# Optimization experiments

Hardware: AMD Instinct MI355X
Metric: run time of the kernel (lower is better)

## Reference

```python
import jax, jax.numpy as jnp
import numpy as np

# Dimensions (see shape_source): batched instruction states.
B, P, D, H, NOPS = 16384, 8, 64, 128, 37
OP_START = 16            # opcode one-hot lives in channels [16, 16+37)
DIV, MOD = 3, 4          # opcode ids for the iterative div/mod paths
CARRY_OPS = (0, 1, 2, 10, 11, 12, 13)  # ADD,SUB,MUL,LT,GT,LE,GE
NITER = 16               # div/mod iteration FFN count (source: ModuleList of 16)
NCASCADE = 7             # carry cascade iterations (source: for _ in range(7))


def setup_inputs() -> dict:
    key = jax.random.key(0)
    ks = jax.random.split(key, 20)
    s = 0.05
    n = lambda k, shape: jax.random.normal(k, shape, dtype=jnp.float32) * s
    return {
        "x": jax.random.normal(ks[0], (B, P, D), dtype=jnp.float32),
        # initial_experts (per-opcode FFN bank)
        "Wi1": n(ks[1], (NOPS, D, H)), "bi1": jnp.zeros((NOPS, H), jnp.float32),
        "Wi2": n(ks[2], (NOPS, H, D)), "bi2": jnp.zeros((NOPS, D), jnp.float32),
        # carry_attn QKV projections
        "Wq": n(ks[3], (D, D)), "Wk": n(ks[4], (D, D)), "Wv": n(ks[5], (D, D)),
        # carry_experts (per-opcode FFN bank used in the 7-iter cascade)
        "Wc1": n(ks[6], (NOPS, D, H)), "bc1": jnp.zeros((NOPS, H), jnp.float32),
        "Wc2": n(ks[7], (NOPS, H, D)), "bc2": jnp.zeros((NOPS, D), jnp.float32),
        # 16 distinct DivIterFFN layers
        "Wd1": n(ks[8], (NITER, D, H)), "bd1": jnp.zeros((NITER, H), jnp.float32),
        "Wd2": n(ks[9], (NITER, H, D)), "bd2": jnp.zeros((NITER, D), jnp.float32),
        # 16 distinct ModIterFFN layers
        "Wm1": n(ks[10], (NITER, D, H)), "bm1": jnp.zeros((NITER, H), jnp.float32),
        "Wm2": n(ks[11], (NITER, H, D)), "bm2": jnp.zeros((NITER, D), jnp.float32),
        # final_experts (per-opcode FFN bank)
        "Wf1": n(ks[12], (NOPS, D, H)), "bf1": jnp.zeros((NOPS, H), jnp.float32),
        "Wf2": n(ks[13], (NOPS, H, D)), "bf2": jnp.zeros((NOPS, D), jnp.float32),
    }


def _moe(x, op, W1, b1, W2, b2):
    """Opcode-routed expert FFN with residual: each batch element uses its opcode's weights."""
    h = jax.nn.relu(jnp.einsum('bpd,bdh->bph', x, W1[op]) + b1[op][:, None, :])
    return x + jnp.einsum('bph,bhd->bpd', h, W2[op]) + b2[op][:, None, :]


def _attn(x, Wq, Wk, Wv):
    """Carry-propagation attention across the 8 nibble positions, residual."""
    q, k, v = x @ Wq, x @ Wk, x @ Wv
    s = jax.nn.softmax(jnp.einsum('bpd,bqd->bpq', q, k) * (1.0 / np.sqrt(D)), axis=-1)
    return x + jnp.einsum('bpq,bqd->bpd', s, v)


def reference(x, Wi1, bi1, Wi2, bi2, Wq, Wk, Wv, Wc1, bc1, Wc2, bc2,
              Wd1, bd1, Wd2, bd2, Wm1, bm1, Wm2, bm2, Wf1, bf1, Wf2, bf2):
    # opcode routing: argmax over the one-hot opcode slice at position 0
    op = jnp.argmax(x[:, 0, OP_START:OP_START + NOPS], axis=-1)  # [B] int
    # Stage 1: initial opcode-routed experts
    x = _moe(x, op, Wi1, bi1, Wi2, bi2)
    carry_mask = jnp.any(op[:, None] == jnp.asarray(CARRY_OPS)[None, :], axis=1)[:, None, None]
    for _ in range(NCASCADE):
        y = _moe(_attn(x, Wq, Wk, Wv), op, Wc1, bc1, Wc2, bc2)
        x = jnp.where(carry_mask, y, x)
    # 16 iterative DIV FFNs (distinct weights per iteration), masked to DIV rows
    div_mask = (op == DIV)[:, None, None]
    for i in range(NITER):
        h = jax.nn.relu(jnp.einsum('bpd,dh->bph', x, Wd1[i]) + bd1[i])
        x = jnp.where(div_mask, x + jnp.einsum('bph,hd->bpd', h, Wd2[i]) + bd2[i], x)
    # 16 iterative MOD FFNs, masked to MOD rows
    mod_mask = (op == MOD)[:, None, None]
    for i in range(NITER):
        h = jax.nn.relu(jnp.einsum('bpd,dh->bph', x, Wm1[i]) + bm1[i])
        x = jnp.where(mod_mask, x + jnp.einsum('bph,hd->bpd', h, Wm2[i]) + bm2[i], x)
    # Stage 4: finalization experts (opcode-routed)
    x = _moe(x, op, Wf1, bf1, Wf2, bf2)
    return x
```

## Files before the change

### kernel.cpp

```cpp
#include <hip/hip_runtime.h>
#include <math.h>


typedef __bf16 bfrag __attribute__((ext_vector_type(8)));
typedef __bf16 bhalf4 __attribute__((ext_vector_type(4)));
typedef float f32x4 __attribute__((ext_vector_type(4)));

#define MFMA16(a,b,c) __builtin_amdgcn_mfma_f32_16x16x32_bf16((a),(b),(c),0,0,0)

constexpr int NB = 16384, NOPS = 37, OP_START = 16;

constexpr int WS_OPARR  = 0;
constexpr int WS_CNT    = 16384;
constexpr int WS_OFF    = 16448;
constexpr int WS_CUR    = 16512;
constexpr int WS_TB     = 16560;
constexpr int WS_ROWIDX = 16640;
constexpr int WS_INTS   = 33024;

constexpr int OFF_QKVT = 0;
constexpr int OFF_WI1T = 12288;
constexpr int OFF_WI2T = 315392;
constexpr int OFF_WC1T = 618496;
constexpr int OFF_WC2T = 921600;
constexpr int OFF_WF1T = 1224704;
constexpr int OFF_WF2T = 1527808;
constexpr int OFF_WD1T = 1830912;
constexpr int OFF_WD2T = 1961984;
constexpr int OFF_WM1T = 2093056;
constexpr int OFF_WM2T = 2224128;


__global__ void k_zero(int* cnt, int* cur) {
    int t = threadIdx.x;
    if (t < NOPS) { cnt[t] = 0; cur[t] = 0; }
}

__global__ void k_op(const float* __restrict__ x, int* __restrict__ opArr, int* __restrict__ cnt) {
    int b = blockIdx.x * 64 + threadIdx.x;
    const float4* p = (const float4*)(x + (size_t)b * 512 + OP_START);
    float best = -1e30f; int op = 0;
    #pragma unroll
    for (int j = 0; j < 9; ++j) {
        float4 v = p[j];
        int k = j * 4;
        if (v.x > best) { best = v.x; op = k; }
        if (v.y > best) { best = v.y; op = k + 1; }
        if (v.z > best) { best = v.z; op = k + 2; }
        if (v.w > best) { best = v.w; op = k + 3; }
    }
    float last = x[(size_t)b * 512 + OP_START + 36];
    if (last > best) op = 36;
    opArr[b] = op;
    atomicAdd(&cnt[op], 1);
}

__global__ void k_scan(const int* __restrict__ cnt, int* __restrict__ off, int* __restrict__ tb) {
    if (threadIdx.x == 0) {
        int a = 0;
        for (int o = 0; o < NOPS; ++o) { off[o] = a; a += cnt[o]; }
        off[NOPS] = a;
        const int pr[9] = {3, 4, 0, 1, 2, 10, 11, 12, 13};
        int t = 0;
        for (int i = 0; i < 9; ++i) { int o = pr[i]; tb[o] = t; t += (cnt[o] + 3) >> 2; }
        for (int o = 0; o < NOPS; ++o) {
            bool heavy = (o <= 4) || (o >= 10 && o <= 13);
            if (heavy) continue;
            tb[o] = t; t += (cnt[o] + 3) >> 2;
        }
        tb[NOPS] = t;
    }
}

__global__ void k_scatter(const int* __restrict__ opArr, const int* __restrict__ off,
                          int* __restrict__ cur, int* __restrict__ rowIdx) {
    __shared__ int h[NOPS], bb[NOPS];
    int tid = threadIdx.x;
    if (tid < NOPS) h[tid] = 0;
    __syncthreads();
    int b = blockIdx.x * 256 + tid;
    int op = opArr[b];
    int my = atomicAdd(&h[op], 1);
    __syncthreads();
    if (tid < NOPS && h[tid] > 0) bb[tid] = atomicAdd(&cur[tid], h[tid]);
    __syncthreads();
    rowIdx[off[op] + bb[op] + my] = b;
}

__global__ void k_tilemap(const int* __restrict__ cnt, const int* __restrict__ tb,
                          int* __restrict__ tileArr) {
    int o = blockIdx.x;
    int n = (cnt[o] + 3) >> 2, base = tb[o];
    for (int t = threadIdx.x; t < n; t += 64)
        tileArr[base + t] = (o << 12) | t;
}

__global__ void k_wt(const float* __restrict__ Wi1, const float* __restrict__ Wi2,
                     const float* __restrict__ Wq,  const float* __restrict__ Wk,
                     const float* __restrict__ Wv,
                     const float* __restrict__ Wc1, const float* __restrict__ Wc2,
                     const float* __restrict__ Wd1, const float* __restrict__ Wd2,
                     const float* __restrict__ Wm1, const float* __restrict__ Wm2,
                     const float* __restrict__ Wf1, const float* __restrict__ Wf2,
                     __bf16* __restrict__ wb) {
    __shared__ float t[8320];
    int m = blockIdx.x;
    const float* src; __bf16* dst; int R, C;
    if      (m < 37)  { src = Wi1 + m * 8192;        dst = wb + OFF_WI1T + m * 8192;        R = 64;  C = 128; }
    else if (m < 74)  { src = Wi2 + (m-37) * 8192;   dst = wb + OFF_WI2T + (m-37) * 8192;   R = 128; C = 64;  }
    else if (m < 111) { src = Wc1 + (m-74) * 8192;   dst = wb + OFF_WC1T + (m-74) * 8192;   R = 64;  C = 128; }
    else if (m < 148) { src = Wc2 + (m-111) * 8192;  dst = wb + OFF_WC2T + (m-111) * 8192;  R = 128; C = 64;  }
    else if (m < 185) { src = Wf1 + (m-148) * 8192;  dst = wb + OFF_WF1T + (m-148) * 8192;  R = 64;  C = 128; }
    else if (m < 222) { src = Wf2 + (m-185) * 8192;  dst = wb + OFF_WF2T + (m-185) * 8192;  R = 128; C = 64;  }
    else if (m < 238) { src = Wd1 + (m-222) * 8192;  dst = wb + OFF_WD1T + (m-222) * 8192;  R = 64;  C = 128; }
    else if (m < 254) { src = Wd2 + (m-238) * 8192;  dst = wb + OFF_WD2T + (m-238) * 8192;  R = 128; C = 64;  }
    else if (m < 270) { src = Wm1 + (m-254) * 8192;  dst = wb + OFF_WM1T + (m-254) * 8192;  R = 64;  C = 128; }
    else if (m < 286) { src = Wm2 + (m-270) * 8192;  dst = wb + OFF_WM2T + (m-270) * 8192;  R = 128; C = 64;  }
    else { const float* q3[3] = {Wq, Wk, Wv}; src = q3[m-286]; dst = wb + OFF_QKVT + (m-286) * 4096; R = 64; C = 64; }
    int n = R * C, Cp = C + 1;
    int logC = (C == 128) ? 7 : 6, logR = (R == 128) ? 7 : 6;
    for (int i = threadIdx.x; i < n; i += 256)
        t[(i >> logC) * Cp + (i & (C - 1))] = src[i];
    __syncthreads();
    for (int o = threadIdx.x; o < n; o += 256) {
        int c = o >> logR, r = o & (R - 1);
        dst[o] = (__bf16)t[r * Cp + c];
    }
}


__device__ __forceinline__ bfrag cvt8(const float* p) {
    float4 a = *(const float4*)p;
    float4 b = *(const float4*)(p + 4);
    bfrag r;
    r[0] = (__bf16)a.x; r[1] = (__bf16)a.y; r[2] = (__bf16)a.z; r[3] = (__bf16)a.w;
    r[4] = (__bf16)b.x; r[5] = (__bf16)b.y; r[6] = (__bf16)b.z; r[7] = (__bf16)b.w;
    return r;
}

__device__ __forceinline__ bhalf4 pack4(f32x4 a) {
    bhalf4 r;
    r[0] = (__bf16)a[0]; r[1] = (__bf16)a[1]; r[2] = (__bf16)a[2]; r[3] = (__bf16)a[3];
    return r;
}

__device__ __forceinline__ bhalf4 pack4_relu(f32x4 a) {
    bhalf4 r;
    r[0] = (__bf16)fmaxf(a[0], 0.0f); r[1] = (__bf16)fmaxf(a[1], 0.0f);
    r[2] = (__bf16)fmaxf(a[2], 0.0f); r[3] = (__bf16)fmaxf(a[3], 0.0f);
    return r;
}

__device__ __forceinline__ void ffn_coop(float* Xs, __bf16* Hs,
    const __bf16* __restrict__ W1t, const float* __restrict__ b1,
    const __bf16* __restrict__ W2t, const float* __restrict__ b2,
    int w, int lq, int qd) {
    __syncthreads();
    {
        bfrag xa[2][2];
        #pragma unroll
        for (int mt = 0; mt < 2; ++mt)
            #pragma unroll
            for (int kf = 0; kf < 2; ++kf)
                xa[mt][kf] = cvt8(&Xs[(mt * 16 + lq) * 68 + kf * 32 + qd * 8]);
        #pragma unroll
        for (int nt2 = 0; nt2 < 2; ++nt2) {
            int nt = w * 2 + nt2;
            float4 bv = *(const float4*)(b1 + nt * 16 + qd * 4);
            f32x4 acc0 = {bv.x, bv.y, bv.z, bv.w}, acc1 = acc0;
            #pragma unroll
            for (int kf = 0; kf < 2; ++kf) {
                bfrag wf = *(const bfrag*)(W1t + (nt * 16 + lq) * 64 + kf * 32 + qd * 8);
                acc0 = MFMA16(wf, xa[0][kf], acc0);
                acc1 = MFMA16(wf, xa[1][kf], acc1);
            }
            *(bhalf4*)&Hs[lq * 136 + nt * 16 + qd * 4]        = pack4_relu(acc0);
            *(bhalf4*)&Hs[(16 + lq) * 136 + nt * 16 + qd * 4] = pack4_relu(acc1);
        }
    }
    __syncthreads();
    {
        float4 bv = *(const float4*)(b2 + w * 16 + qd * 4);
        f32x4 acc0 = {bv.x, bv.y, bv.z, bv.w}, acc1 = acc0;
        #pragma unroll
        for (int kf = 0; kf < 4; ++kf) {
            bfrag wf = *(const bfrag*)(W2t + (w * 16 + lq) * 128 + kf * 32 + qd * 8);
            bfrag h0 = *(const bfrag*)&Hs[lq * 136 + kf * 32 + qd * 8];
            bfrag h1 = *(const bfrag*)&Hs[(16 + lq) * 136 + kf * 32 + qd * 8];
            acc0 = MFMA16(wf, h0, acc0);
            acc1 = MFMA16(wf, h1, acc1);
        }
        float4* p0 = (float4*)&Xs[lq * 68 + w * 16 + qd * 4];
        float4 v0 = *p0;
        v0.x += acc0[0]; v0.y += acc0[1]; v0.z += acc0[2]; v0.w += acc0[3];
        *p0 = v0;
        float4* p1 = (float4*)&Xs[(16 + lq) * 68 + w * 16 + qd * 4];
        float4 v1 = *p1;
        v1.x += acc1[0]; v1.y += acc1[1]; v1.z += acc1[2]; v1.w += acc1[3];
        *p1 = v1;
    }
}

__device__ __forceinline__ void attn_coop(float* Xs, __bf16* Qb, __bf16* Kb,
    __bf16* VtT, __bf16* Pb, const __bf16* __restrict__ qkvt, int w, int lq, int qd) {
    int c = w >> 1, half = w & 1;
    __syncthreads();
    {
        bfrag xa[2];
        #pragma unroll
        for (int kf = 0; kf < 2; ++kf)
            xa[kf] = cvt8(&Xs[(c * 16 + lq) * 68 + kf * 32 + qd * 8]);
        int nt0 = half * 6;
        #pragma unroll
        for (int i = 0; i < 6; ++i) {
            int nt = nt0 + i;
            f32x4 acc = {0.f, 0.f, 0.f, 0.f};
            if (nt < 8) {
                #pragma unroll
                for (int kf = 0; kf < 2; ++kf) {
                    bfrag wf = *(const bfrag*)(qkvt + (nt * 16 + lq) * 64 + kf * 32 + qd * 8);
                    acc = MFMA16(wf, xa[kf], acc);
                }
                __bf16* dst = (nt < 4)
                    ? &Qb[c * 1280 + lq * 80 + nt * 16 + qd * 4]
                    : &Kb[c * 1280 + lq * 80 + (nt - 4) * 16 + qd * 4];
                *(bhalf4*)dst = pack4(acc);
            } else {
                #pragma unroll
                for (int kf = 0; kf < 2; ++kf) {
                    bfrag wf = *(const bfrag*)(qkvt + (nt * 16 + lq) * 64 + kf * 32 + qd * 8);
                    acc = MFMA16(xa[kf], wf, acc);
                }
                *(bhalf4*)&VtT[c * 2048 + ((nt - 8) * 16 + lq) * 32 + qd * 4] = pack4(acc);
            }
        }
    }
    __syncthreads();
    {
        f32x4 sv = {0.f, 0.f, 0.f, 0.f};
        #pragma unroll
        for (int kf = 0; kf < 2; ++kf) {
            bfrag qa = *(const bfrag*)&Qb[c * 1280 + (half * 8 + lq) * 80 + kf * 32 + qd * 8];
            bfrag kb = *(const bfrag*)&Kb[c * 1280 + (half * 8 + lq) * 80 + kf * 32 + qd * 8];
            sv = MFMA16(qa, kb, sv);
        }
        float p4[4];
        #pragma unroll
        for (int r = 0; r < 4; ++r) {
            float v = sv[r] * 0.125f;
            float m = v;
            m = fmaxf(m, __shfl_xor(m, 1));
            m = fmaxf(m, __shfl_xor(m, 2));
            m = fmaxf(m, __shfl_xor(m, 4));
            float e = __expf(v - m);
            float s = e;
            s += __shfl_xor(s, 1);
            s += __shfl_xor(s, 2);
            s += __shfl_xor(s, 4);
            p4[r] = e * __builtin_amdgcn_rcpf(s);
        }
        if (lq < 8 && qd < 2) {
            #pragma unroll
            for (int r = 0; r < 4; ++r)
                Pb[c * 512 + (half * 8 + qd * 4 + r) * 32 + half * 8 + lq] = (__bf16)p4[r];
        }
    }
    __syncthreads();
    {
        bfrag pb = *(const bfrag*)&Pb[c * 512 + lq * 32 + qd * 8];
        #pragma unroll
        for (int i = 0; i < 2; ++i) {
            int nt = half * 2 + i;
            bfrag va = *(const bfrag*)&VtT[c * 2048 + (nt * 16 + lq) * 32 + qd * 8];
            f32x4 z = {0.f, 0.f, 0.f, 0.f};
            f32x4 acc = MFMA16(va, pb, z);
            float4* xp = (float4*)&Xs[(c * 16 + lq) * 68 + nt * 16 + qd * 4];
            float4 xv = *xp;
            xv.x += acc[0]; xv.y += acc[1]; xv.z += acc[2]; xv.w += acc[3];
            *xp = xv;
        }
    }
}


__global__ void __launch_bounds__(256, 4)
moe_main(const float* __restrict__ x, float* __restrict__ out,
         const int* __restrict__ tileArr, const int* __restrict__ tb,
         const int* __restrict__ cnt, const int* __restrict__ off,
         const int* __restrict__ rowIdx, const __bf16* __restrict__ wb,
         const float* __restrict__ bi1, const float* __restrict__ bi2,
         const float* __restrict__ bc1, const float* __restrict__ bc2,
         const float* __restrict__ bd1, const float* __restrict__ bd2,
         const float* __restrict__ bm1, const float* __restrict__ bm2,
         const float* __restrict__ bf1_, const float* __restrict__ bf2_) {
    __shared__ float Xs[32 * 68];
    __shared__ __align__(16) unsigned char UB[20480];
    __bf16* Hs  = (__bf16*)UB;
    __bf16* Qb  = (__bf16*)UB;
    __bf16* Kb  = (__bf16*)(UB + 5120);
    __bf16* VtT = (__bf16*)(UB + 10240);
    __bf16* Pb  = (__bf16*)(UB + 18432);

    int g = blockIdx.x;
    if (g >= tb[NOPS]) return;
    int v = tileArr[g];
    int op = v >> 12, tile = v & 4095;

    int tid = threadIdx.x;
    int w = tid >> 6, lane = tid & 63, lq = lane & 15, qd = lane >> 4;

    int base = off[op] + tile * 4;
    int nr = cnt[op] - tile * 4; if (nr > 4) nr = 4;
    int rows[4];
    #pragma unroll
    for (int s = 0; s < 4; ++s) rows[s] = rowIdx[base + (s < nr ? s : nr - 1)];

    bool carry = (op <= 2) || (op >= 10 && op <= 13);

    for (int i = tid; i < 2048; i += 256) {
        int m = i >> 6, d = i & 63;
        Xs[m * 68 + d] = x[(size_t)rows[m >> 3] * 512 + (m & 7) * 64 + d];
    }
    if (carry) {
        for (int i = tid; i < 1024; i += 256) Pb[i] = (__bf16)0.0f;
        for (int i = tid; i < 2048; i += 256) {
            int c2 = i >> 10, rem = i & 1023, d = rem >> 4, p = rem & 15;
            VtT[c2 * 2048 + d * 32 + 16 + p] = (__bf16)0.0f;
        }
    }

    ffn_coop(Xs, Hs, wb + OFF_WI1T + op * 8192, bi1 + op * 128,
                     wb + OFF_WI2T + op * 8192, bi2 + op * 64, w, lq, qd);

    if (carry) {
        const __bf16* qkvt = wb + OFF_QKVT;
        for (int it = 0; it < 7; ++it) {
            attn_coop(Xs, Qb, Kb, VtT, Pb, qkvt, w, lq, qd);
            ffn_coop(Xs, Hs, wb + OFF_WC1T + op * 8192, bc1 + op * 128,
                             wb + OFF_WC2T + op * 8192, bc2 + op * 64, w, lq, qd);
        }
    }
    if (op == 3) {
        for (int i = 0; i < 16; ++i)
            ffn_coop(Xs, Hs, wb + OFF_WD1T + i * 8192, bd1 + i * 128,
                             wb + OFF_WD2T + i * 8192, bd2 + i * 64, w, lq, qd);
    }
    if (op == 4) {
        for (int i = 0; i < 16; ++i)
            ffn_coop(Xs, Hs, wb + OFF_WM1T + i * 8192, bm1 + i * 128,
                             wb + OFF_WM2T + i * 8192, bm2 + i * 64, w, lq, qd);
    }
    ffn_coop(Xs, Hs, wb + OFF_WF1T + op * 8192, bf1_ + op * 128,
                     wb + OFF_WF2T + op * 8192, bf2_ + op * 64, w, lq, qd);

    __syncthreads();
    for (int i = tid; i < nr * 512; i += 256) {
        int s = i >> 9, rem = i & 511;
        out[(size_t)rows[s] * 512 + rem] = Xs[(s * 8 + (rem >> 6)) * 68 + (rem & 63)];
    }
}


extern "C" void kernel_launch(void* const* d_in, const int* in_sizes, int n_in,
                              void* d_out, int out_size, void* d_ws, size_t ws_size,
                              hipStream_t stream) {
    (void)in_sizes; (void)n_in; (void)out_size; (void)ws_size;
    const float* x   = (const float*)d_in[0];
    const float* Wi1 = (const float*)d_in[1];
    const float* bi1 = (const float*)d_in[2];
    const float* Wi2 = (const float*)d_in[3];
    const float* bi2 = (const float*)d_in[4];
    const float* Wq  = (const float*)d_in[5];
    const float* Wk  = (const float*)d_in[6];
    const float* Wv  = (const float*)d_in[7];
    const float* Wc1 = (const float*)d_in[8];
    const float* bc1 = (const float*)d_in[9];
    const float* Wc2 = (const float*)d_in[10];
    const float* bc2 = (const float*)d_in[11];
    const float* Wd1 = (const float*)d_in[12];
    const float* bd1 = (const float*)d_in[13];
    const float* Wd2 = (const float*)d_in[14];
    const float* bd2 = (const float*)d_in[15];
    const float* Wm1 = (const float*)d_in[16];
    const float* bm1 = (const float*)d_in[17];
    const float* Wm2 = (const float*)d_in[18];
    const float* bm2 = (const float*)d_in[19];
    const float* Wf1 = (const float*)d_in[20];
    const float* bf1 = (const float*)d_in[21];
    const float* Wf2 = (const float*)d_in[22];
    const float* bf2 = (const float*)d_in[23];
    float* out = (float*)d_out;

    int* wsi     = (int*)d_ws;
    int* opArr   = wsi + WS_OPARR;
    int* tileArr = wsi + WS_OPARR;
    int* cnt     = wsi + WS_CNT;
    int* off     = wsi + WS_OFF;
    int* cur     = wsi + WS_CUR;
    int* tb      = wsi + WS_TB;
    int* rowIdx  = wsi + WS_ROWIDX;
    __bf16* wb   = (__bf16*)((char*)d_ws + WS_INTS * 4);

    k_zero<<<1, 64, 0, stream>>>(cnt, cur);
    k_op<<<NB / 64, 64, 0, stream>>>(x, opArr, cnt);
    k_scan<<<1, 64, 0, stream>>>(cnt, off, tb);
    k_scatter<<<NB / 256, 256, 0, stream>>>(opArr, off, cur, rowIdx);
    k_tilemap<<<NOPS, 64, 0, stream>>>(cnt, tb, tileArr);
    k_wt<<<289, 256, 0, stream>>>(Wi1, Wi2, Wq, Wk, Wv, Wc1, Wc2, Wd1, Wd2, Wm1, Wm2, Wf1, Wf2, wb);
    moe_main<<<NB / 4 + NOPS, 256, 0, stream>>>(x, out, tileArr, tb, cnt, off, rowIdx, wb,
                                                bi1, bi2, bc1, bc2, bd1, bd2, bm1, bm2, bf1, bf2);
}
```

Measured before the change: 275.0 us.

## Prefetch FFN/attn weights before barriers, vectorize row I/O, parallelize scan

Weight and bias fragments for each FFN and attention stage are now loaded into registers before the leading barrier, so global load latency can overlap synchronisation. Row gather into shared memory and the output store use float4 accesses instead of scalar ones. The single-thread scan is replaced by a wavefront shuffle scan that also resets the cursor array. The zeroing kernel becomes a memset. Extra live registers may lower occupancy.

```diff
diff --git a/kernel.cpp b/kernel.cpp
--- a/kernel.cpp
+++ b/kernel.cpp
@@ -31,11 +31,6 @@
 constexpr int OFF_WM2T = 2224128;
 
 
-__global__ void k_zero(int* cnt, int* cur) {
-    int t = threadIdx.x;
-    if (t < NOPS) { cnt[t] = 0; cur[t] = 0; }
-}
-
 __global__ void k_op(const float* __restrict__ x, int* __restrict__ opArr, int* __restrict__ cnt) {
     int b = blockIdx.x * 64 + threadIdx.x;
     const float4* p = (const float4*)(x + (size_t)b * 512 + OP_START);
@@ -55,21 +50,43 @@
     atomicAdd(&cnt[op], 1);
 }
 
-__global__ void k_scan(const int* __restrict__ cnt, int* __restrict__ off, int* __restrict__ tb) {
-    if (threadIdx.x == 0) {
-        int a = 0;
-        for (int o = 0; o < NOPS; ++o) { off[o] = a; a += cnt[o]; }
-        off[NOPS] = a;
-        const int pr[9] = {3, 4, 0, 1, 2, 10, 11, 12, 13};
-        int t = 0;
-        for (int i = 0; i < 9; ++i) { int o = pr[i]; tb[o] = t; t += (cnt[o] + 3) >> 2; }
-        for (int o = 0; o < NOPS; ++o) {
-            bool heavy = (o <= 4) || (o >= 10 && o <= 13);
-            if (heavy) continue;
-            tb[o] = t; t += (cnt[o] + 3) >> 2;
-        }
-        tb[NOPS] = t;
-    }
+__device__ __forceinline__ int rank_of(int o) {
+    if (o == 3 || o == 4) return o - 3;
+    if (o <= 2) return o + 2;
+    if (o >= 10 && o <= 13) return o - 5;
+    if (o <= 9) return o + 4;
+    return o;
+}
+
+__global__ void k_scan(const int* __restrict__ cnt, int* __restrict__ off,
+                       int* __restrict__ tb, int* __restrict__ cur) {
+    __shared__ int srt[64], pre[64];
+    int t = threadIdx.x;
+    int c = (t < NOPS) ? cnt[t] : 0;
+    int inc = c;
+    #pragma unroll
+    for (int d = 1; d < 64; d <<= 1) {
+        int v = __shfl_up(inc, d);
+        if (t >= d) inc += v;
+    }
+    if (t < NOPS) { off[t] = inc - c; cur[t] = 0; }
+    if (t == NOPS - 1) off[NOPS] = inc;
+    int tc = (c + 3) >> 2;
+    srt[t] = 0;
+    __syncthreads();
+    if (t < NOPS) srt[rank_of(t)] = tc;
+    __syncthreads();
+    int s = srt[t];
+    int sinc = s;
+    #pragma unroll
+    for (int d = 1; d < 64; d <<= 1) {
+        int v = __shfl_up(sinc, d);
+        if (t >= d) sinc += v;
+    }
+    pre[t] = sinc - s;
+    if (t == 63) tb[NOPS] = sinc;
+    __syncthreads();
+    if (t < NOPS) tb[t] = pre[rank_of(t)];
 }
 
 __global__ void k_scatter(const int* __restrict__ opArr, const int* __restrict__ off,
@@ -155,6 +172,19 @@
     const __bf16* __restrict__ W1t, const float* __restrict__ b1,
     const __bf16* __restrict__ W2t, const float* __restrict__ b2,
     int w, int lq, int qd) {
+    bfrag w1f[2][2], w2f[4];
+    #pragma unroll
+    for (int nt2 = 0; nt2 < 2; ++nt2)
+        #pragma unroll
+        for (int kf = 0; kf < 2; ++kf)
+            w1f[nt2][kf] = *(const bfrag*)(W1t + ((w * 2 + nt2) * 16 + lq) * 64 + kf * 32 + qd * 8);
+    #pragma unroll
+    for (int kf = 0; kf < 4; ++kf)
+        w2f[kf] = *(const bfrag*)(W2t + (w * 16 + lq) * 128 + kf * 32 + qd * 8);
+    float4 b1v[2];
+    b1v[0] = *(const float4*)(b1 + (w * 2 + 0) * 16 + qd * 4);
+    b1v[1] = *(const float4*)(b1 + (w * 2 + 1) * 16 + qd * 4);
+    float4 b2v = *(const float4*)(b2 + w * 16 + qd * 4);
     __syncthreads();
     {
         bfrag xa[2][2];
@@ -166,13 +196,11 @@
         #pragma unroll
         for (int nt2 = 0; nt2 < 2; ++nt2) {
             int nt = w * 2 + nt2;
-            float4 bv = *(const float4*)(b1 + nt * 16 + qd * 4);
-            f32x4 acc0 = {bv.x, bv.y, bv.z, bv.w}, acc1 = acc0;
+            f32x4 acc0 = {b1v[nt2].x, b1v[nt2].y, b1v[nt2].z, b1v[nt2].w}, acc1 = acc0;
             #pragma unroll
             for (int kf = 0; kf < 2; ++kf) {
-                bfrag wf = *(const bfrag*)(W1t + (nt * 16 + lq) * 64 + kf * 32 + qd * 8);
-                acc0 = MFMA16(wf, xa[0][kf], acc0);
-                acc1 = MFMA16(wf, xa[1][kf], acc1);
+                acc0 = MFMA16(w1f[nt2][kf], xa[0][kf], acc0);
+                acc1 = MFMA16(w1f[nt2][kf], xa[1][kf], acc1);
             }
             *(bhalf4*)&Hs[lq * 136 + nt * 16 + qd * 4]        = pack4_relu(acc0);
             *(bhalf4*)&Hs[(16 + lq) * 136 + nt * 16 + qd * 4] = pack4_relu(acc1);
@@ -180,15 +208,13 @@
     }
     __syncthreads();
     {
-        float4 bv = *(const float4*)(b2 + w * 16 + qd * 4);
-        f32x4 acc0 = {bv.x, bv.y, bv.z, bv.w}, acc1 = acc0;
+        f32x4 acc0 = {b2v.x, b2v.y, b2v.z, b2v.w}, acc1 = acc0;
         #pragma unroll
         for (int kf = 0; kf < 4; ++kf) {
-            bfrag wf = *(const bfrag*)(W2t + (w * 16 + lq) * 128 + kf * 32 + qd * 8);
             bfrag h0 = *(const bfrag*)&Hs[lq * 136 + kf * 32 + qd * 8];
             bfrag h1 = *(const bfrag*)&Hs[(16 + lq) * 136 + kf * 32 + qd * 8];
-            acc0 = MFMA16(wf, h0, acc0);
-            acc1 = MFMA16(wf, h1, acc1);
+            acc0 = MFMA16(w2f[kf], h0, acc0);
+            acc1 = MFMA16(w2f[kf], h1, acc1);
         }
         float4* p0 = (float4*)&Xs[lq * 68 + w * 16 + qd * 4];
         float4 v0 = *p0;
@@ -204,6 +230,14 @@
 __device__ __forceinline__ void attn_coop(float* Xs, __bf16* Qb, __bf16* Kb,
     __bf16* VtT, __bf16* Pb, const __bf16* __restrict__ qkvt, int w, int lq, int qd) {
     int c = w >> 1, half = w & 1;
+    bfrag wfp[6][2];
+    #pragma unroll
+    for (int i = 0; i < 6; ++i) {
+        int nt = half * 6 + i;
+        #pragma unroll
+        for (int kf = 0; kf < 2; ++kf)
+            wfp[i][kf] = *(const bfrag*)(qkvt + (nt * 16 + lq) * 64 + kf * 32 + qd * 8);
+    }
     __syncthreads();
     {
         bfrag xa[2];
@@ -217,20 +251,16 @@
             f32x4 acc = {0.f, 0.f, 0.f, 0.f};
             if (nt < 8) {
                 #pragma unroll
-                for (int kf = 0; kf < 2; ++kf) {
-                    bfrag wf = *(const bfrag*)(qkvt + (nt * 16 + lq) * 64 + kf * 32 + qd * 8);
-                    acc = MFMA16(wf, xa[kf], acc);
-                }
+                for (int kf = 0; kf < 2; ++kf)
+                    acc = MFMA16(wfp[i][kf], xa[kf], acc);
                 __bf16* dst = (nt < 4)
                     ? &Qb[c * 1280 + lq * 80 + nt * 16 + qd * 4]
                     : &Kb[c * 1280 + lq * 80 + (nt - 4) * 16 + qd * 4];
                 *(bhalf4*)dst = pack4(acc);
             } else {
                 #pragma unroll
-                for (int kf = 0; kf < 2; ++kf) {
-                    bfrag wf = *(const bfrag*)(qkvt + (nt * 16 + lq) * 64 + kf * 32 + qd * 8);
-                    acc = MFMA16(xa[kf], wf, acc);
-                }
+                for (int kf = 0; kf < 2; ++kf)
+                    acc = MFMA16(xa[kf], wfp[i][kf], acc);
                 *(bhalf4*)&VtT[c * 2048 + ((nt - 8) * 16 + lq) * 32 + qd * 4] = pack4(acc);
             }
         }
@@ -317,9 +347,12 @@
 
     bool carry = (op <= 2) || (op >= 10 && op <= 13);
 
-    for (int i = tid; i < 2048; i += 256) {
-        int m = i >> 6, d = i & 63;
-        Xs[m * 68 + d] = x[(size_t)rows[m >> 3] * 512 + (m & 7) * 64 + d];
+    {
+        int i0 = tid * 8;
+        int m = i0 >> 6, d = i0 & 63;
+        const float* srcp = x + (size_t)rows[m >> 3] * 512 + (m & 7) * 64 + d;
+        *(float4*)&Xs[m * 68 + d]     = *(const float4*)srcp;
+        *(float4*)&Xs[m * 68 + d + 4] = *(const float4*)(srcp + 4);
     }
     if (carry) {
         for (int i = tid; i < 1024; i += 256) Pb[i] = (__bf16)0.0f;
@@ -354,9 +387,10 @@
                      wb + OFF_WF2T + op * 8192, bf2_ + op * 64, w, lq, qd);
 
     __syncthreads();
-    for (int i = tid; i < nr * 512; i += 256) {
+    for (int i = tid * 4; i < nr * 512; i += 1024) {
         int s = i >> 9, rem = i & 511;
-        out[(size_t)rows[s] * 512 + rem] = Xs[(s * 8 + (rem >> 6)) * 68 + (rem & 63)];
+        *(float4*)&out[(size_t)rows[s] * 512 + rem] =
+            *(float4*)&Xs[(s * 8 + (rem >> 6)) * 68 + (rem & 63)];
     }
 }
 
@@ -401,9 +435,9 @@
     int* rowIdx  = wsi + WS_ROWIDX;
     __bf16* wb   = (__bf16*)((char*)d_ws + WS_INTS * 4);
 
-    k_zero<<<1, 64, 0, stream>>>(cnt, cur);
+    hipMemsetAsync((char*)d_ws + WS_CNT * 4, 0, NOPS * 4, stream);
     k_op<<<NB / 64, 64, 0, stream>>>(x, opArr, cnt);
-    k_scan<<<1, 64, 0, stream>>>(cnt, off, tb);
+    k_scan<<<1, 64, 0, stream>>>(cnt, off, tb, cur);
     k_scatter<<<NB / 256, 256, 0, stream>>>(opArr, off, cur, rowIdx);
     k_tilemap<<<NOPS, 64, 0, stream>>>(cnt, tb, tileArr);
     k_wt<<<289, 256, 0, stream>>>(Wi1, Wi2, Wq, Wk, Wv, Wc1, Wc2, Wd1, Wd2, Wm1, Wm2, Wf1, Wf2, wb);
```

Result: faster. 265.7 us (-3.4%).
